# Optimization experiments

Hardware: AMD Instinct MI355X
Metric: run time of the kernel (lower is better)

## Reference

```python
import jax, jax.numpy as jnp
import numpy as np

B = 16384
IN = 1024
H = 1024
LN_EPS = 1e-5


def setup_inputs() -> dict:
    key = jax.random.key(0)
    ks = jax.random.split(key, 8)
    # Five gate Linears fused into one weight [IN+H, 5H] (order: f, i, o, c, m)
    scale = 1.0 / np.sqrt(IN + H)
    W = jax.random.uniform(ks[0], (IN + H, 5 * H), jnp.float32, -scale, scale)
    b = jax.random.uniform(ks[1], (5 * H,), jnp.float32, -scale, scale)
    return {
        "x": jax.random.normal(ks[2], (B, IN), jnp.float32),
        "h_prev": jax.random.normal(ks[3], (B, H), jnp.float32),
        "c_prev": jax.random.normal(ks[4], (B, H), jnp.float32),
        "W": W,
        "b": b,
        "ln_gamma": jnp.ones((H,), jnp.float32),
        "ln_beta": jnp.zeros((H,), jnp.float32),
        "retention": jnp.full((H,), 0.9, jnp.float32),
    }


def _layernorm(z, gamma, beta):
    mu = jnp.mean(z, axis=-1, keepdims=True)
    var = jnp.var(z, axis=-1, keepdims=True)
    return (z - mu) * jax.lax.rsqrt(var + LN_EPS) * gamma + beta


def reference(x, h_prev, c_prev, W, b, ln_gamma, ln_beta, retention):
    combined = jnp.concatenate([x, h_prev], axis=-1)        # [B, IN+H]
    gates = combined @ W + b                                # [B, 5H] fused GEMM
    f_pre, i_pre, o_pre, c_pre_act, m_pre = jnp.split(gates, 5, axis=-1)
    f_gate = jax.nn.sigmoid(f_pre)
    i_gate = jax.nn.sigmoid(i_pre)
    o_gate = jax.nn.sigmoid(o_pre)
    c_cand = jnp.tanh(c_pre_act)
    m_gate = jax.nn.sigmoid(m_pre)
    c_new = f_gate * c_prev + i_gate * c_cand
    c_new = c_new * retention + (1.0 - retention) * c_prev
    c_new = m_gate * c_new + (1.0 - m_gate) * c_prev
    # exp(ln)/(1+exp(ln)) == sigmoid(layernorm(o_gate))
    o_exp = jax.nn.sigmoid(_layernorm(o_gate, ln_gamma, ln_beta))
    h_new = o_exp * jnp.tanh(c_new)
    return h_new, c_new
```

## Files before the change

kernel.cpp:

```cpp
#include <hip/hip_runtime.h>
#include <math.h>


typedef unsigned short u16;
typedef unsigned int   u32;
typedef short  short8 __attribute__((ext_vector_type(8)));
typedef float  f32x4  __attribute__((ext_vector_type(4)));
typedef u16    u16x4  __attribute__((ext_vector_type(4)));
typedef u32    u32x4  __attribute__((ext_vector_type(4)));

#define B_ROWS 16384
#define K_DIM  2048
#define N_DIM  5120
#define H_DIM  1024

__device__ __forceinline__ float b2f(u16 u) {
    u32 v = ((u32)u) << 16;
    return __uint_as_float(v);
}
__device__ __forceinline__ u16 f2b(float f) {
    u32 x = __float_as_uint(f);
    u32 r = (x + 0x7fffu + ((x >> 16) & 1u)) >> 16;
    return (u16)r;
}
__device__ __forceinline__ float sigm(float v) {
    return 1.f / (1.f + __expf(-v));
}
__device__ __forceinline__ float tanh_fast(float v) {
    v = fminf(fmaxf(v, -15.f), 15.f);
    float e = __expf(-2.f * v);
    return (1.f - e) / (1.f + e);
}

__global__ __launch_bounds__(256) void convert_A(const float* __restrict__ x,
                                                 const float* __restrict__ h,
                                                 u16* __restrict__ A) {
    size_t idx = ((size_t)blockIdx.x * 256 + threadIdx.x) * 8;
    int row = (int)(idx >> 11);
    int col = (int)(idx & 2047);
    int srcCol = (col & ~63) | (((((col >> 3) & 7) ^ (row & 7))) << 3);
    const float* src = (srcCol < 1024) ? (x + (size_t)row * 1024 + srcCol)
                                       : (h + (size_t)row * 1024 + (srcCol - 1024));
    f32x4 v0 = *(const f32x4*)src;
    f32x4 v1 = *(const f32x4*)(src + 4);
    u32x4 w;
    w.x = (u32)f2b(v0.x) | ((u32)f2b(v0.y) << 16);
    w.y = (u32)f2b(v0.z) | ((u32)f2b(v0.w) << 16);
    w.z = (u32)f2b(v1.x) | ((u32)f2b(v1.y) << 16);
    w.w = (u32)f2b(v1.z) | ((u32)f2b(v1.w) << 16);
    *(u32x4*)(A + idx) = w;
}

__global__ __launch_bounds__(256) void convert_W(const float* __restrict__ W,
                                                 u16* __restrict__ Wt) {
    __shared__ float tile[64][33];
    const int t  = threadIdx.x;
    const int tx = t & 31;
    const int ty = t >> 5;
    const int n0 = blockIdx.x * 32;
    const int k0 = blockIdx.y * 64;
#pragma unroll
    for (int i = 0; i < 8; ++i)
        tile[ty + 8 * i][tx] = W[(size_t)(k0 + ty + 8 * i) * N_DIM + n0 + tx];
    __syncthreads();
    const int n = t >> 3;
    const int s = t & 7;
    const int g = s ^ (n & 7);
    u32x4 w;
    w.x = (u32)f2b(tile[g * 8 + 0][n]) | ((u32)f2b(tile[g * 8 + 1][n]) << 16);
    w.y = (u32)f2b(tile[g * 8 + 2][n]) | ((u32)f2b(tile[g * 8 + 3][n]) << 16);
    w.z = (u32)f2b(tile[g * 8 + 4][n]) | ((u32)f2b(tile[g * 8 + 5][n]) << 16);
    w.w = (u32)f2b(tile[g * 8 + 6][n]) | ((u32)f2b(tile[g * 8 + 7][n]) << 16);
    *(u32x4*)(Wt + (size_t)(n0 + n) * K_DIM + k0 + s * 8) = w;
}

#define BK 64

__device__ __forceinline__ void gld_lds16(const void* g, void* l) {
    __builtin_amdgcn_global_load_lds(
        (const __attribute__((address_space(1))) void*)g,
        (__attribute__((address_space(3))) void*)l, 16, 0, 0);
}

#define AU(s, h) ((s) * 16384 + (h) * 8192)
#define BU(s, h) (32768 + (s) * 16384 + (h) * 8192)

#define SBAR()  __builtin_amdgcn_sched_barrier(0)
#define BAR()   do { SBAR(); asm volatile("s_barrier" ::: "memory"); SBAR(); } while (0)
#define LGKM0() do { asm volatile("s_waitcnt lgkmcnt(0)" ::: "memory"); SBAR(); } while (0)
#define VM4()   asm volatile("s_waitcnt vmcnt(4)" ::: "memory")

__global__ __launch_bounds__(512, 2) void gemm_gates(const u16* __restrict__ A,
                                                     const u16* __restrict__ Bt,
                                                     const float* __restrict__ bias,
                                                     u16* __restrict__ gates) {
    __shared__ u16 lds[65536];

    const int t = threadIdx.x;
    const int bid = blockIdx.x;
    const int swz = (bid & 7) * 160 + (bid >> 3);
    const int m0 = (swz & 63) << 8;
    const int n0 = (swz >> 6) << 8;

    const int l   = t & 63;
    const int wid = t >> 6;
    const int wr  = wid >> 2;
    const int wc  = wid & 3;
    const int lr  = l & 15;
    const int lh  = l >> 4;
    const int z   = lr & 7;
    const int sA0 = (lh ^ z) * 8;

    const int tb = t >> 3;
    const u16* aBase = A  + (size_t)(m0 + tb) * K_DIM + (t & 7) * 8;
    const u16* bBase = Bt + (size_t)(n0 + (tb & 31) + (tb >> 5) * 64) * K_DIM
                          + (t & 7) * 8;
    const int dOff = t * 8;

    f32x4 acc[8][4] = {};
    short8 af[4][2], bf0[2][2], bf1[2][2];

#define STAGE_A(s, h, OFF) do {                                               \
    gld_lds16(aBase + (size_t)((h) * 64) * K_DIM + (OFF),                     \
              &lds[AU(s, h) + dOff]);                                         \
    gld_lds16(aBase + (size_t)((h) * 64 + 128) * K_DIM + (OFF),               \
              &lds[AU(s, h) + 4096 + dOff]);                                  \
} while (0)
#define STAGE_B(s, h, OFF) do {                                               \
    gld_lds16(bBase + (size_t)((h) * 32) * K_DIM + (OFF),                     \
              &lds[BU(s, h) + dOff]);                                         \
    gld_lds16(bBase + (size_t)((h) * 32 + 128) * K_DIM + (OFF),               \
              &lds[BU(s, h) + 4096 + dOff]);                                  \
} while (0)

#define RD_AF(s, q) do {                                                      \
    _Pragma("unroll") for (int m = 0; m < 4; ++m) {                           \
        const int u_ = AU(s, q) + (wr * 64 + m * 16 + lr) * 64;               \
        af[m][0] = *(const short8*)&lds[u_ + sA0];                            \
        af[m][1] = *(const short8*)&lds[u_ + (sA0 ^ 32)];                     \
    }                                                                         \
} while (0)
#define RD_BF(dst, s, h) do {                                                 \
    _Pragma("unroll") for (int n = 0; n < 2; ++n) {                           \
        const int u_ = BU(s, h) + (wc * 32 + n * 16 + lr) * 64;               \
        dst[n][0] = *(const short8*)&lds[u_ + sA0];                           \
        dst[n][1] = *(const short8*)&lds[u_ + (sA0 ^ 32)];                    \
    }                                                                         \
} while (0)

#define MFMA16(q, nh, BF) do {                                                \
    __builtin_amdgcn_s_setprio(1);                                            \
    _Pragma("unroll") for (int sk = 0; sk < 2; ++sk)                          \
    _Pragma("unroll") for (int m = 0; m < 4; ++m)                             \
    _Pragma("unroll") for (int n = 0; n < 2; ++n)                             \
        acc[(q) * 4 + m][(nh) * 2 + n] =                                      \
            __builtin_amdgcn_mfma_f32_16x16x32_bf16(                          \
                af[m][sk], BF[n][sk], acc[(q) * 4 + m][(nh) * 2 + n], 0, 0, 0);\
    __builtin_amdgcn_s_setprio(0);                                            \
} while (0)

    STAGE_A(0, 0, 0); STAGE_B(0, 0, 0); STAGE_B(0, 1, 0); STAGE_A(0, 1, 0);
    SBAR(); VM4(); BAR();

#pragma unroll 1
    for (int kt = 0; kt < 32; ++kt) {
        const int s  = kt & 1;
        const int sp = s ^ 1;
        const int OFF = (kt + 1) * BK;
        RD_AF(s, 0); RD_BF(bf0, s, 0); STAGE_A(sp, 0, OFF);
        BAR(); LGKM0(); MFMA16(0, 0, bf0);
        VM4();
        BAR();
        RD_BF(bf1, s, 1); STAGE_B(sp, 0, OFF);
        BAR(); LGKM0(); MFMA16(0, 1, bf1);
        VM4();
        BAR();
        RD_AF(s, 1); STAGE_B(sp, 1, OFF);
        BAR(); LGKM0(); MFMA16(1, 1, bf1);
        BAR();
        STAGE_A(sp, 1, OFF);
        BAR(); MFMA16(1, 0, bf0);
        VM4();
        BAR();
    }
#undef STAGE_A
#undef STAGE_B
#undef RD_AF
#undef RD_BF
#undef MFMA16

    const int grp = n0 >> 10;
#pragma unroll
    for (int ni = 0; ni < 4; ++ni) {
        int col = n0 + wc * 64 + ni * 16 + lr;
        float bv = bias[col];
#pragma unroll
        for (int q = 0; q < 2; ++q) {
#pragma unroll
            for (int m = 0; m < 4; ++m) {
#pragma unroll
                for (int j = 0; j < 4; ++j) {
                    int row = m0 + wr * 128 + q * 64 + m * 16 + lh * 4 + j;
                    float v = acc[q * 4 + m][ni][j] + bv;
                    float g = (grp == 3) ? tanh_fast(v) : sigm(v);
                    gates[(size_t)row * N_DIM + col] = f2b(g);
                }
            }
        }
    }
}

__global__ __launch_bounds__(256) void fuse_out(const u16* __restrict__ gates,
                                                const float* __restrict__ c_prev,
                                                const float* __restrict__ ret,
                                                const float* __restrict__ gamma,
                                                const float* __restrict__ beta,
                                                float* __restrict__ out) {
    const int r = blockIdx.x;
    const int t = threadIdx.x;
    const u16* g = gates + (size_t)r * N_DIM;
    const int j0 = t * 4;

    u16x4 ov = *(const u16x4*)(g + 2048 + j0);
    float o0 = b2f(ov.x), o1 = b2f(ov.y), o2 = b2f(ov.z), o3 = b2f(ov.w);
    float s1 = o0 + o1 + o2 + o3;
    float s2 = o0 * o0 + o1 * o1 + o2 * o2 + o3 * o3;
#pragma unroll
    for (int off = 32; off; off >>= 1) {
        s1 += __shfl_xor(s1, off, 64);
        s2 += __shfl_xor(s2, off, 64);
    }
    __shared__ float red[8];
    if ((t & 63) == 0) { red[t >> 6] = s1; red[4 + (t >> 6)] = s2; }
    __syncthreads();
    float S1 = red[0] + red[1] + red[2] + red[3];
    float S2 = red[4] + red[5] + red[6] + red[7];
    float mu   = S1 * (1.f / 1024.f);
    float var  = S2 * (1.f / 1024.f) - mu * mu;
    float rstd = rsqrtf(var + 1e-5f);

    u16x4 fv = *(const u16x4*)(g + j0);
    u16x4 iv = *(const u16x4*)(g + 1024 + j0);
    u16x4 cv = *(const u16x4*)(g + 3072 + j0);
    u16x4 mv = *(const u16x4*)(g + 4096 + j0);
    f32x4 cp = *(const f32x4*)(c_prev + (size_t)r * H_DIM + j0);
    f32x4 rt = *(const f32x4*)(ret + j0);
    f32x4 gm = *(const f32x4*)(gamma + j0);
    f32x4 bt = *(const f32x4*)(beta + j0);

    float of[4] = {o0, o1, o2, o3};
    u16 fa[4] = {fv.x, fv.y, fv.z, fv.w};
    u16 ia[4] = {iv.x, iv.y, iv.z, iv.w};
    u16 ca[4] = {cv.x, cv.y, cv.z, cv.w};
    u16 ma[4] = {mv.x, mv.y, mv.z, mv.w};

    f32x4 hout, cout;
#pragma unroll
    for (int i = 0; i < 4; ++i) {
        float f = b2f(fa[i]), ig = b2f(ia[i]), cc = b2f(ca[i]), m = b2f(ma[i]);
        float cpv = cp[i], rv = rt[i];
        float c1 = f * cpv + ig * cc;
        float c2 = c1 * rv + (1.f - rv) * cpv;
        float cn = m * c2 + (1.f - m) * cpv;
        float ln = (of[i] - mu) * rstd * gm[i] + bt[i];
        float oe = sigm(ln);
        float hn = oe * tanh_fast(cn);
        hout[i] = hn;
        cout[i] = cn;
    }
    *(f32x4*)(out + (size_t)r * H_DIM + j0) = hout;
    *(f32x4*)(out + (size_t)B_ROWS * H_DIM + (size_t)r * H_DIM + j0) = cout;
}

extern "C" void kernel_launch(void* const* d_in, const int* in_sizes, int n_in,
                              void* d_out, int out_size, void* d_ws, size_t ws_size,
                              hipStream_t stream) {
    const float* x      = (const float*)d_in[0];
    const float* h_prev = (const float*)d_in[1];
    const float* c_prev = (const float*)d_in[2];
    const float* W      = (const float*)d_in[3];
    const float* bias   = (const float*)d_in[4];
    const float* gamma  = (const float*)d_in[5];
    const float* beta   = (const float*)d_in[6];
    const float* ret    = (const float*)d_in[7];
    float* out = (float*)d_out;

    u16* Abuf  = (u16*)d_ws;
    u16* Wt    = Abuf + (size_t)B_ROWS * K_DIM;
    u16* gates = Wt + (size_t)N_DIM * K_DIM;

    convert_A<<<(B_ROWS * K_DIM / 8) / 256, 256, 0, stream>>>(x, h_prev, Abuf);
    convert_W<<<dim3(N_DIM / 32, K_DIM / 64), 256, 0, stream>>>(W, Wt);
    gemm_gates<<<(B_ROWS / 256) * (N_DIM / 256), 512, 0, stream>>>(Abuf, Wt, bias, gates);
    fuse_out<<<B_ROWS, 256, 0, stream>>>(gates, c_prev, ret, gamma, beta, out);
}
```

Baseline: 486.7 us.

## Stage GEMM epilogue through swizzled LDS for coalesced 16-byte gate stores

The GEMM epilogue now writes activated bf16 gate values into a swizzled LDS tile, then has each thread copy 16-byte vectors of whole rows to global memory. This replaces the scattered 2-byte stores to global memory. The main loop also drops the explicit lgkmcnt(0) waits and switches to the builtin s_barrier, leaving the compiler to insert LDS waits itself. The cost is extra LDS traffic and two block-wide syncs in the epilogue, plus some risk around how the compiler orders LDS waits.

```diff
diff --git a/kernel.cpp b/kernel.cpp
--- a/kernel.cpp
+++ b/kernel.cpp
@@ -7,6 +7,7 @@
 typedef short  short8 __attribute__((ext_vector_type(8)));
 typedef float  f32x4  __attribute__((ext_vector_type(4)));
 typedef u16    u16x4  __attribute__((ext_vector_type(4)));
+typedef u16    u16x8  __attribute__((ext_vector_type(8)));
 typedef u32    u32x4  __attribute__((ext_vector_type(4)));
 
 #define B_ROWS 16384
@@ -85,10 +86,10 @@
 #define AU(s, h) ((s) * 16384 + (h) * 8192)
 #define BU(s, h) (32768 + (s) * 16384 + (h) * 8192)
 
-#define SBAR()  __builtin_amdgcn_sched_barrier(0)
-#define BAR()   do { SBAR(); asm volatile("s_barrier" ::: "memory"); SBAR(); } while (0)
-#define LGKM0() do { asm volatile("s_waitcnt lgkmcnt(0)" ::: "memory"); SBAR(); } while (0)
-#define VM4()   asm volatile("s_waitcnt vmcnt(4)" ::: "memory")
+#define BAR() do { __builtin_amdgcn_sched_barrier(0);                         \
+                   __builtin_amdgcn_s_barrier();                              \
+                   __builtin_amdgcn_sched_barrier(0); } while (0)
+#define VM4() asm volatile("s_waitcnt vmcnt(4)" ::: "memory")
 
 __global__ __launch_bounds__(512, 2) void gemm_gates(const u16* __restrict__ A,
                                                      const u16* __restrict__ Bt,
@@ -160,7 +161,9 @@
 } while (0)
 
     STAGE_A(0, 0, 0); STAGE_B(0, 0, 0); STAGE_B(0, 1, 0); STAGE_A(0, 1, 0);
-    SBAR(); VM4(); BAR();
+    __builtin_amdgcn_sched_barrier(0);
+    VM4();
+    BAR();
 
 #pragma unroll 1
     for (int kt = 0; kt < 32; ++kt) {
@@ -168,46 +171,56 @@
         const int sp = s ^ 1;
         const int OFF = (kt + 1) * BK;
         RD_AF(s, 0); RD_BF(bf0, s, 0); STAGE_A(sp, 0, OFF);
-        BAR(); LGKM0(); MFMA16(0, 0, bf0);
-        VM4();
-        BAR();
+        BAR(); MFMA16(0, 0, bf0); VM4(); BAR();
         RD_BF(bf1, s, 1); STAGE_B(sp, 0, OFF);
-        BAR(); LGKM0(); MFMA16(0, 1, bf1);
-        VM4();
-        BAR();
+        BAR(); MFMA16(0, 1, bf1); VM4(); BAR();
         RD_AF(s, 1); STAGE_B(sp, 1, OFF);
-        BAR(); LGKM0(); MFMA16(1, 1, bf1);
-        BAR();
+        BAR(); MFMA16(1, 1, bf1); BAR();
         STAGE_A(sp, 1, OFF);
-        BAR(); MFMA16(1, 0, bf0);
-        VM4();
-        BAR();
+        BAR(); MFMA16(1, 0, bf0); VM4(); BAR();
     }
 #undef STAGE_A
 #undef STAGE_B
+
+    asm volatile("s_waitcnt vmcnt(0)" ::: "memory");
+    __syncthreads();
+
+    const int grp = n0 >> 10;
+    float bv[4];
+#pragma unroll
+    for (int ni = 0; ni < 4; ++ni) bv[ni] = bias[n0 + wc * 64 + ni * 16 + lr];
+
+#pragma unroll
+    for (int q = 0; q < 2; ++q) {
+#pragma unroll
+        for (int m = 0; m < 4; ++m) {
+#pragma unroll
+            for (int ni = 0; ni < 4; ++ni) {
+#pragma unroll
+                for (int j = 0; j < 4; ++j) {
+                    int r = wr * 128 + q * 64 + m * 16 + lh * 4 + j;
+                    int c = wc * 64 + ni * 16 + lr;
+                    float v = acc[q * 4 + m][ni][j] + bv[ni];
+                    float g = (grp == 3) ? tanh_fast(v) : sigm(v);
+                    lds[r * 256 + ((((c >> 3) ^ (r & 31))) << 3) + (c & 7)] = f2b(g);
+                }
+            }
+        }
+    }
+    __syncthreads();
+
+    const int r0 = t >> 1;
+    const int ch = (t & 1) * 128;
+    u16* dst = gates + (size_t)(m0 + r0) * N_DIM + n0 + ch;
+#pragma unroll
+    for (int k = 0; k < 16; ++k) {
+        int gidx = (ch >> 3) + k;
+        u16x8 v = *(const u16x8*)&lds[r0 * 256 + ((gidx ^ (r0 & 31)) << 3)];
+        *(u16x8*)(dst + k * 8) = v;
+    }
 #undef RD_AF
 #undef RD_BF
 #undef MFMA16
-
-    const int grp = n0 >> 10;
-#pragma unroll
-    for (int ni = 0; ni < 4; ++ni) {
-        int col = n0 + wc * 64 + ni * 16 + lr;
-        float bv = bias[col];
-#pragma unroll
-        for (int q = 0; q < 2; ++q) {
-#pragma unroll
-            for (int m = 0; m < 4; ++m) {
-#pragma unroll
-                for (int j = 0; j < 4; ++j) {
-                    int row = m0 + wr * 128 + q * 64 + m * 16 + lh * 4 + j;
-                    float v = acc[q * 4 + m][ni][j] + bv;
-                    float g = (grp == 3) ? tanh_fast(v) : sigm(v);
-                    gates[(size_t)row * N_DIM + col] = f2b(g);
-                }
-            }
-        }
-    }
 }
 
 __global__ __launch_bounds__(256) void fuse_out(const u16* __restrict__ gates,
```

Result: no change. 494.4 us (+1.6%).
